# Optimization experiments

Measured on AMD Instinct MI355X. Metric: run time of the kernel, lower is better.

## Reference

```python
import jax, jax.numpy as jnp
import numpy as np

EPS = 1e-5

def _layernorm(x, w, b):
    # x: [B, L, C]; WithBias_LayerNorm over last dim (biased variance)
    mu = jnp.mean(x, axis=-1, keepdims=True)
    var = jnp.mean((x - mu) ** 2, axis=-1, keepdims=True)
    return (x - mu) / jnp.sqrt(var + EPS) * w + b

def _selective_scan(x, x_proj_w, dt_w, A_logs, Ds):
    # x: [B, D, L]  (D = ssm d_inner = 192, N = d_state = 16, R = dt_rank = 6)
    Bsz, D, L = x.shape
    N = A_logs.shape[1]
    R = dt_w.shape[1]
    x_dbl = jnp.einsum('bdl,rd->blr', x, x_proj_w)            # [B, L, R+2N]
    dts_r = x_dbl[..., :R]
    Bs = x_dbl[..., R:R + N]                                   # [B, L, N]
    Cs = x_dbl[..., R + N:]                                    # [B, L, N]
    dts = jax.nn.softplus(jnp.einsum('blr,dr->bld', dts_r, dt_w))  # [B, L, D]
    As = -jnp.exp(A_logs.astype(jnp.float32))                  # [D, N]
    dt_A = jnp.exp(jnp.einsum('bld,dn->bldn', dts, As))        # [B, L, D, N]
    dt_B_x = jnp.einsum('bld,bln,bdl->bldn', dts, Bs, x)       # [B, L, D, N]

    def step(u, inp):
        a, bx, c = inp                                         # [B,D,N],[B,D,N],[B,N]
        u = a * u + bx
        y = jnp.einsum('bdn,bn->bd', u, c)
        return u, y

    u0 = jnp.zeros((Bsz, D, N), dtype=jnp.float32)
    _, ys = jax.lax.scan(step, u0, (jnp.swapaxes(dt_A, 0, 1),
                                     jnp.swapaxes(dt_B_x, 0, 1),
                                     jnp.swapaxes(Cs, 0, 1)))
    y = jnp.swapaxes(ys, 0, 1)                                 # [B, L, D]
    y = y + jnp.einsum('bdl,d->bld', x, Ds.astype(jnp.float32))
    return y


def setup_inputs() -> dict:
    key = jax.random.key(0)
    ks = jax.random.split(key, 12)
    B, C, H, W = 64, 2048, 24, 8
    D_in2, Dssm, N, R = 384, 192, 16, 6
    s = 0.02
    return {
        'feat_map': jax.random.normal(ks[0], (B, C, H, W), jnp.float32),
        'ln_w': jnp.ones((C,), jnp.float32),
        'ln_b': jnp.zeros((C,), jnp.float32),
        'in_w': jax.random.normal(ks[1], (D_in2, C), jnp.float32) * s,
        'in_b': jnp.zeros((D_in2,), jnp.float32),
        'x_proj_w': jax.random.normal(ks[2], (R + 2 * N, Dssm), jnp.float32) * s,
        'dt_w': jax.random.normal(ks[3], (Dssm, R), jnp.float32) * 0.1,
        'A_logs': jnp.log(jnp.broadcast_to(jnp.arange(1, N + 1, dtype=jnp.float32), (Dssm, N))),
        'Ds': jnp.ones((Dssm,), jnp.float32),
        'out_w': jax.random.normal(ks[4], (C, Dssm), jnp.float32) * s,
        'out_b': jnp.zeros((C,), jnp.float32),
        'mo_w': jax.random.normal(ks[5], (C, C), jnp.float32) * s,
        'mo_b': jnp.zeros((C,), jnp.float32),
        'bn_w': jnp.ones((C,), jnp.float32),
        'bn_b': jnp.zeros((C,), jnp.float32),
        'bn_rm': jax.random.normal(ks[6], (C,), jnp.float32) * 0.1,
        'bn_rv': jax.random.uniform(ks[7], (C,), jnp.float32) + 0.5,
    }


def reference(feat_map, ln_w, ln_b, in_w, in_b, x_proj_w, dt_w, A_logs, Ds,
              out_w, out_b, mo_w, mo_b, bn_w, bn_b, bn_rm, bn_rv):
    B, C, H, W = feat_map.shape
    L = H * W
    x3 = feat_map.transpose(0, 2, 3, 1).reshape(B, L, C)       # to_3d
    fm = _layernorm(x3, ln_w, ln_b)                            # normalized feat_map [B, L, C]
    xz = jnp.einsum('blc,oc->blo', fm, in_w) + in_b            # 1x1 conv in_proj
    x, z = jnp.split(xz, 2, axis=-1)                           # each [B, L, 192]
    xd = jnp.swapaxes(x, 1, 2)                                 # [B, D, L]
    yf = _selective_scan(xd, x_proj_w, dt_w, A_logs, Ds)       # [B, L, D]
    yb = _selective_scan(xd[:, :, ::-1], x_proj_w, dt_w, A_logs, Ds)[:, ::-1, :]
    ssm = yf + yb                                              # [B, L, D]
    ssm = ssm * jax.nn.silu(z)
    out = jnp.einsum('bld,cd->blc', ssm, out_w) + out_b        # out_proj 1x1 conv
    out = out + fm                                             # drop_path is identity at eval
    out = jnp.einsum('blc,oc->blo', out, mo_w) + mo_b          # mamba_out conv 1x1
    out = (out - bn_rm) / jnp.sqrt(bn_rv + EPS) * bn_w + bn_b  # BatchNorm (eval)
    out = jax.nn.relu(out)
    return out.reshape(B, H, W, C).transpose(0, 3, 1, 2)
```

## Files before the change

### kernel.cpp

```cpp
#include <hip/hip_runtime.h>
#include <math.h>

#define EPSV 1e-5f


typedef __attribute__((ext_vector_type(8))) __bf16 bf16x8;
typedef __attribute__((ext_vector_type(4))) float f32x4;

__device__ __forceinline__ ushort f2bf(float f) {
  union { float f; unsigned u; } v; v.f = f;
  const unsigned r = v.u + 0x7fffu + ((v.u >> 16) & 1u);
  return (ushort)(r >> 16);
}

#define GLOAD16(G, L) __builtin_amdgcn_global_load_lds( \
    (__attribute__((address_space(1))) void*)(G), \
    (__attribute__((address_space(3))) void*)(L), 16, 0, 0)

__global__ __launch_bounds__(256) void cvt_kernel(
    const float* __restrict__ s, ushort* __restrict__ d, int n)
{
  const int i = (blockIdx.x * 256 + threadIdx.x) * 4;
  if (i + 3 < n) {
    const float4 v = *(const float4*)(s + i);
    ushort4 o;
    o.x = f2bf(v.x); o.y = f2bf(v.y); o.z = f2bf(v.z); o.w = f2bf(v.w);
    *(ushort4*)(d + i) = o;
  }
}

__global__ __launch_bounds__(256) void transpose_w(
    const float* __restrict__ w, ushort* __restrict__ wT)
{
  __shared__ float t[64][65];
  const int c0 = blockIdx.x * 64, d0 = blockIdx.y * 64;
  const int tl = threadIdx.x & 63, tg = threadIdx.x >> 6;
#pragma unroll
  for (int r = 0; r < 16; ++r) {
    const int c = r * 4 + tg;
    t[c][tl] = w[(size_t)(c0 + c) * 192 + d0 + tl];
  }
  __syncthreads();
#pragma unroll
  for (int r = 0; r < 16; ++r) {
    const int d = r * 4 + tg;
    wT[(size_t)(d0 + d) * 2048 + c0 + tl] = f2bf(t[tl][d]);
  }
}

__global__ __launch_bounds__(256) void ln_stats(
    const float* __restrict__ feat, float* __restrict__ sums)
{
  const int b = blockIdx.x, c0 = blockIdx.y * 128;
  const int l = threadIdx.x;
  if (l >= 192) return;
  const float* p = feat + ((size_t)b * 2048 + c0) * 192 + l;
  float s = 0.f, sq = 0.f;
  for (int c = 0; c < 128; ++c) { const float v = p[(size_t)c * 192]; s += v; sq = fmaf(v, v, sq); }
  atomicAdd(&sums[(b * 192 + l) * 2], s);
  atomicAdd(&sums[(b * 192 + l) * 2 + 1], sq);
}

__global__ __launch_bounds__(256) void ln_apply(
    const float* __restrict__ feat, const float* __restrict__ sums,
    const float* __restrict__ lnw, const float* __restrict__ lnb,
    ushort* __restrict__ fm)
{
  __shared__ float tile[64][65];
  __shared__ float smu[64], srs[64];
  const int b = blockIdx.x, c0 = blockIdx.y * 64, l0 = blockIdx.z * 64;
  const int tl = threadIdx.x & 63, tg = threadIdx.x >> 6;
#pragma unroll
  for (int r = 0; r < 16; ++r) {
    const int c = r * 4 + tg;
    tile[c][tl] = feat[((size_t)b * 2048 + c0 + c) * 192 + l0 + tl];
  }
  if (threadIdx.x < 64) {
    const float s  = sums[(b * 192 + l0 + threadIdx.x) * 2];
    const float sq = sums[(b * 192 + l0 + threadIdx.x) * 2 + 1];
    const float mu = s * (1.f / 2048.f);
    smu[threadIdx.x] = mu;
    srs[threadIdx.x] = rsqrtf(sq * (1.f / 2048.f) - mu * mu + EPSV);
  }
  __syncthreads();
  const float w = lnw[c0 + tl], bb = lnb[c0 + tl];
#pragma unroll
  for (int r = 0; r < 16; ++r) {
    const int ll = r * 4 + tg;
    fm[((size_t)(b * 192 + l0 + ll)) * 2048 + c0 + tl] =
        f2bf((tile[tl][ll] - smu[ll]) * srs[ll] * w + bb);
  }
}

__device__ __forceinline__ void mfma_phase(
    const ushort* __restrict__ Ag, int lda,
    const ushort* __restrict__ Bg, int ldb, int K,
    int bm, int bn, int tid, ushort* As, ushort* Bs, f32x4 acc[4][4])
{
  const int lane = tid & 63, wave = tid >> 6;
  const int wm = (wave & 1) << 6, wn = (wave >> 1) << 6;
  const int fr = lane & 15, q = lane >> 4;
  const int r0 = tid >> 2, kc = (tid & 3) << 3;
  const int lb = (tid & 192) * 8;
  for (int k0 = 0; k0 < K; k0 += 32) {
    __syncthreads();
    GLOAD16(Ag + (size_t)(bm + r0) * lda + k0 + kc,      As + lb);
    GLOAD16(Ag + (size_t)(bm + 64 + r0) * lda + k0 + kc, As + 2048 + lb);
    GLOAD16(Bg + (size_t)(bn + r0) * ldb + k0 + kc,      Bs + lb);
    GLOAD16(Bg + (size_t)(bn + 64 + r0) * ldb + k0 + kc, Bs + 2048 + lb);
    __syncthreads();
    bf16x8 af[4], bfr[4];
#pragma unroll
    for (int i = 0; i < 4; ++i) {
      af[i]  = *(const bf16x8*)&As[(wm + i * 16 + fr) * 32 + q * 8];
      bfr[i] = *(const bf16x8*)&Bs[(wn + i * 16 + fr) * 32 + q * 8];
    }
#pragma unroll
    for (int i = 0; i < 4; ++i)
#pragma unroll
      for (int j = 0; j < 4; ++j)
        acc[i][j] = __builtin_amdgcn_mfma_f32_16x16x32_bf16(af[i], bfr[j], acc[i][j], 0, 0, 0);
  }
}

template<int MODE>
__global__ __launch_bounds__(256) void mfma_gemm(
    const ushort* __restrict__ A1, const ushort* __restrict__ B1,
    const ushort* __restrict__ A2, const ushort* __restrict__ B2,
    const float* __restrict__ p0, const float* __restrict__ p1,
    float* __restrict__ out, ushort* __restrict__ outb)
{
  __shared__ ushort As[4096], Bs[4096];
  const int tid = threadIdx.x;
  const int bm = blockIdx.y * 128, bn = blockIdx.x * 128;
  f32x4 acc[4][4];
#pragma unroll
  for (int i = 0; i < 4; ++i)
#pragma unroll
    for (int j = 0; j < 4; ++j) acc[i][j] = (f32x4)(0.f);

  mfma_phase(A1, 2048, B1, 2048, 2048, bm, bn, tid, As, Bs, acc);
  if (MODE == 1)
    mfma_phase(A2, 192, B2, 192, 192, bm, bn, tid, As, Bs, acc);

  const int lane = tid & 63, wave = tid >> 6;
  const int wm = (wave & 1) << 6, wn = (wave >> 1) << 6;
  const int fr = lane & 15, q = lane >> 4;
  if (MODE == 0) {
#pragma unroll
    for (int mi = 0; mi < 4; ++mi) {
      const int m0 = bm + wm + mi * 16 + q * 4;
#pragma unroll
      for (int ni = 0; ni < 4; ++ni) {
        const int n = bn + wn + ni * 16 + fr;
        const float bias = p0[n];
#pragma unroll
        for (int r = 0; r < 4; ++r)
          out[(size_t)(m0 + r) * 384 + n] = acc[mi][ni][r] + bias;
      }
    }
  } else if (MODE == 1) {
#pragma unroll
    for (int mi = 0; mi < 4; ++mi) {
      const int m0 = bm + wm + mi * 16 + q * 4;
      const int b = m0 / 192, l0 = m0 - b * 192;
#pragma unroll
      for (int ni = 0; ni < 4; ++ni) {
        const int n = bn + wn + ni * 16 + fr;
        const float sc = p0[n], sh = p1[n];
        float4 o;
        o.x = fmaxf(fmaf(acc[mi][ni][0], sc, sh), 0.f);
        o.y = fmaxf(fmaf(acc[mi][ni][1], sc, sh), 0.f);
        o.z = fmaxf(fmaf(acc[mi][ni][2], sc, sh), 0.f);
        o.w = fmaxf(fmaf(acc[mi][ni][3], sc, sh), 0.f);
        *(float4*)(out + ((size_t)b * 2048 + n) * 192 + l0) = o;
      }
    }
  } else {
#pragma unroll
    for (int mi = 0; mi < 4; ++mi) {
      const int m0 = bm + wm + mi * 16 + q * 4;
#pragma unroll
      for (int ni = 0; ni < 4; ++ni) {
        const int n = bn + wn + ni * 16 + fr;
        if (n < 192) {
#pragma unroll
          for (int r = 0; r < 4; ++r)
            outb[(size_t)(m0 + r) * 192 + n] = f2bf(acc[mi][ni][r]);
        }
      }
    }
  }
}

__global__ __launch_bounds__(64) void xproj_kernel(
    const float* __restrict__ xz, const float* __restrict__ xpw,
    const float* __restrict__ dtw, float* __restrict__ dts,
    float* __restrict__ Bsb, float* __restrict__ Csb)
{
  const int m = blockIdx.x, tid = threadIdx.x;
  __shared__ float xrow[192];
  __shared__ float xdbl[38];
  const float* src = xz + (size_t)m * 384;
#pragma unroll
  for (int i = 0; i < 3; ++i) xrow[tid + i * 64] = src[tid + i * 64];
  __syncthreads();
  if (tid < 38) {
    float a = 0.f;
    const float* wr = xpw + tid * 192;
    for (int d = 0; d < 192; ++d) a = fmaf(xrow[d], wr[d], a);
    xdbl[tid] = a;
  }
  __syncthreads();
  if (tid < 16) Bsb[(size_t)m * 16 + tid] = xdbl[6 + tid];
  else if (tid < 32) Csb[(size_t)m * 16 + (tid - 16)] = xdbl[22 + (tid - 16)];
#pragma unroll
  for (int i = 0; i < 3; ++i) {
    const int d = tid + i * 64;
    const float* w = dtw + d * 6;
    float a = xdbl[0] * w[0] + xdbl[1] * w[1] + xdbl[2] * w[2]
            + xdbl[3] * w[3] + xdbl[4] * w[4] + xdbl[5] * w[5];
    dts[(size_t)m * 192 + d] = (a > 20.f) ? a : log1pf(__expf(a));
  }
}

__global__ __launch_bounds__(256) void scan_kernel(
    const float* __restrict__ xz, const float* __restrict__ dts,
    const float* __restrict__ Bsb, const float* __restrict__ Csb,
    const float* __restrict__ A_logs, const float* __restrict__ Ds,
    ushort* __restrict__ ssm)
{
  __shared__ float s_dt[3072], s_x[3072], s_B[3072], s_C[3072], s_y[3072];
  const int tid = threadIdx.x;
  const int b = blockIdx.x / 12, dblk = blockIdx.x - b * 12;
  const int d0 = dblk * 16;
  const size_t rbase = (size_t)b * 192;
  for (int i = tid; i < 768; i += 256) {
    const int l = i >> 2, j = (i & 3) << 2;
    const size_t row = rbase + l;
    ((float4*)s_dt)[i] = *(const float4*)(dts + row * 192 + d0 + j);
    ((float4*)s_x)[i]  = *(const float4*)(xz  + row * 384 + d0 + j);
    ((float4*)s_B)[i]  = *(const float4*)(Bsb + row * 16 + j);
    ((float4*)s_C)[i]  = *(const float4*)(Csb + row * 16 + j);
  }
  __syncthreads();
  const int n = tid & 15, dl = tid >> 4;
  const float Acoef = -expf(A_logs[(d0 + dl) * 16 + n]);
  float u = 0.f;
#pragma unroll 4
  for (int l = 0; l < 192; ++l) {
    const float dt = s_dt[l * 16 + dl];
    const float c  = dt * s_B[l * 16 + n] * s_x[l * 16 + dl];
    const float a  = __expf(dt * Acoef);
    u = fmaf(a, u, c);
    float y = u * s_C[l * 16 + n];
    y += __shfl_xor(y, 1, 16); y += __shfl_xor(y, 2, 16);
    y += __shfl_xor(y, 4, 16); y += __shfl_xor(y, 8, 16);
    if (n == 0) s_y[l * 16 + dl] = y;
  }
  u = 0.f;
#pragma unroll 4
  for (int l = 191; l >= 0; --l) {
    const float dt = s_dt[l * 16 + dl];
    const float c  = dt * s_B[l * 16 + n] * s_x[l * 16 + dl];
    const float a  = __expf(dt * Acoef);
    u = fmaf(a, u, c);
    float y = u * s_C[l * 16 + n];
    y += __shfl_xor(y, 1, 16); y += __shfl_xor(y, 2, 16);
    y += __shfl_xor(y, 4, 16); y += __shfl_xor(y, 8, 16);
    if (n == 0) s_y[l * 16 + dl] += y;
  }
  __syncthreads();
  for (int i = tid; i < 768; i += 256) {
    const int l = i >> 2, j = (i & 3) << 2;
    const size_t row = rbase + l;
    const float4 y4 = ((const float4*)s_y)[i];
    const float4 x4 = ((const float4*)s_x)[i];
    const float4 z4 = *(const float4*)(xz + row * 384 + 192 + d0 + j);
    const float4 D4 = *(const float4*)(Ds + d0 + j);
    ushort4 o;
    o.x = f2bf((y4.x + 2.f * x4.x * D4.x) * (z4.x / (1.f + __expf(-z4.x))));
    o.y = f2bf((y4.y + 2.f * x4.y * D4.y) * (z4.y / (1.f + __expf(-z4.y))));
    o.z = f2bf((y4.z + 2.f * x4.z * D4.z) * (z4.z / (1.f + __expf(-z4.z))));
    o.w = f2bf((y4.w + 2.f * x4.w * D4.w) * (z4.w / (1.f + __expf(-z4.w))));
    *(ushort4*)(ssm + row * 192 + d0 + j) = o;
  }
}

__global__ __launch_bounds__(64) void prep_kernel(
    const float* __restrict__ mo_w, const float* __restrict__ mo_b,
    const float* __restrict__ out_b,
    const float* __restrict__ bn_w, const float* __restrict__ bn_b,
    const float* __restrict__ bn_rm, const float* __restrict__ bn_rv,
    float* __restrict__ scale, float* __restrict__ shift)
{
  const int o = blockIdx.x, tid = threadIdx.x;
  float s = 0.f;
  for (int c = tid; c < 2048; c += 64) s = fmaf(mo_w[(size_t)o * 2048 + c], out_b[c], s);
#pragma unroll
  for (int off = 32; off > 0; off >>= 1) s += __shfl_down(s, off, 64);
  if (tid == 0) {
    const float b2 = s + mo_b[o];
    const float sc = bn_w[o] * rsqrtf(bn_rv[o] + EPSV);
    scale[o] = sc;
    shift[o] = (b2 - bn_rm[o]) * sc + bn_b[o];
  }
}

extern "C" void kernel_launch(void* const* d_in, const int* in_sizes, int n_in,
                              void* d_out, int out_size, void* d_ws, size_t ws_size,
                              hipStream_t stream) {
  const float* feat  = (const float*)d_in[0];
  const float* ln_w  = (const float*)d_in[1];
  const float* ln_b  = (const float*)d_in[2];
  const float* in_w  = (const float*)d_in[3];
  const float* in_b  = (const float*)d_in[4];
  const float* xpw   = (const float*)d_in[5];
  const float* dtw   = (const float*)d_in[6];
  const float* A_logs= (const float*)d_in[7];
  const float* Ds    = (const float*)d_in[8];
  const float* out_w = (const float*)d_in[9];
  const float* out_b = (const float*)d_in[10];
  const float* mo_w  = (const float*)d_in[11];
  const float* mo_b  = (const float*)d_in[12];
  const float* bn_w  = (const float*)d_in[13];
  const float* bn_b  = (const float*)d_in[14];
  const float* bn_rm = (const float*)d_in[15];
  const float* bn_rv = (const float*)d_in[16];
  float* out = (float*)d_out;

  uint8_t* p = (uint8_t*)d_ws;
  ushort* fm_b  = (ushort*)p; p += (size_t)12288 * 2048 * 2;
  float*  xz    = (float*)p;  p += (size_t)12288 * 384 * 4;
  float*  dts   = (float*)p;  p += (size_t)12288 * 192 * 4;
  float*  Bsb   = (float*)p;  p += (size_t)12288 * 16 * 4;
  float*  Csb   = (float*)p;  p += (size_t)12288 * 16 * 4;
  ushort* ssm_b = (ushort*)p; p += (size_t)12288 * 192 * 2;
  ushort* W2b   = (ushort*)p; p += (size_t)2048 * 192 * 2;
  ushort* owT_b = (ushort*)p; p += (size_t)256 * 2048 * 2;
  ushort* mo_wb = (ushort*)p; p += (size_t)2048 * 2048 * 2;
  ushort* in_wb = (ushort*)p; p += (size_t)384 * 2048 * 2;
  float*  scale = (float*)p;  p += 2048 * 4;
  float*  shift = (float*)p;  p += 2048 * 4;
  float*  sums  = (float*)p;  p += (size_t)64 * 192 * 2 * 4;
  if ((size_t)(p - (uint8_t*)d_ws) > ws_size) return;

  cvt_kernel<<<4096, 256, 0, stream>>>(mo_w, mo_wb, 2048 * 2048);
  cvt_kernel<<<768, 256, 0, stream>>>(in_w, in_wb, 384 * 2048);
  hipMemsetAsync(owT_b, 0, (size_t)256 * 2048 * 2, stream);
  transpose_w<<<dim3(32, 3), 256, 0, stream>>>(out_w, owT_b);

  hipMemsetAsync(sums, 0, (size_t)64 * 192 * 2 * 4, stream);
  ln_stats<<<dim3(64, 16), 256, 0, stream>>>(feat, sums);
  ln_apply<<<dim3(64, 32, 3), 256, 0, stream>>>(feat, sums, ln_w, ln_b, fm_b);

  mfma_gemm<0><<<dim3(3, 96), 256, 0, stream>>>(
      fm_b, in_wb, nullptr, nullptr, in_b, nullptr, xz, nullptr);

  xproj_kernel<<<12288, 64, 0, stream>>>(xz, xpw, dtw, dts, Bsb, Csb);
  scan_kernel<<<768, 256, 0, stream>>>(xz, dts, Bsb, Csb, A_logs, Ds, ssm_b);

  mfma_gemm<2><<<dim3(2, 16), 256, 0, stream>>>(
      mo_wb, owT_b, nullptr, nullptr, nullptr, nullptr, nullptr, W2b);
  prep_kernel<<<2048, 64, 0, stream>>>(mo_w, mo_b, out_b, bn_w, bn_b, bn_rm, bn_rv, scale, shift);

  mfma_gemm<1><<<dim3(16, 96), 256, 0, stream>>>(
      fm_b, mo_wb, ssm_b, W2b, scale, shift, out, nullptr);
}
```

Baseline: 717.3 us.

## Replace final fused GEMM with larger-tile double-buffered MFMA kernel

The final 12288x2048x2240 GEMM (fm·mo_w plus ssm·W2) moves from a 128x128 single-buffered kernel to a dedicated 192x256 tile kernel with 512 threads. It uses global_load_lds prefetch two K-steps ahead into double-buffered, XOR-swizzled LDS, and raises wave priority around the MFMA bursts. The aim is more data reuse per tile, less LDS bank conflicting, and overlap of loads with compute. In exchange it uses much more LDS and registers per block, which may limit occupancy, and the hand-written waitcnt and barrier schedule is fragile.

```diff
diff --git a/kernel.cpp b/kernel.cpp
--- a/kernel.cpp
+++ b/kernel.cpp
@@ -126,8 +126,7 @@
 template<int MODE>
 __global__ __launch_bounds__(256) void mfma_gemm(
     const ushort* __restrict__ A1, const ushort* __restrict__ B1,
-    const ushort* __restrict__ A2, const ushort* __restrict__ B2,
-    const float* __restrict__ p0, const float* __restrict__ p1,
+    const float* __restrict__ p0,
     float* __restrict__ out, ushort* __restrict__ outb)
 {
   __shared__ ushort As[4096], Bs[4096];
@@ -140,8 +139,6 @@
     for (int j = 0; j < 4; ++j) acc[i][j] = (f32x4)(0.f);
 
   mfma_phase(A1, 2048, B1, 2048, 2048, bm, bn, tid, As, Bs, acc);
-  if (MODE == 1)
-    mfma_phase(A2, 192, B2, 192, 192, bm, bn, tid, As, Bs, acc);
 
   const int lane = tid & 63, wave = tid >> 6;
   const int wm = (wave & 1) << 6, wn = (wave >> 1) << 6;
@@ -159,23 +156,6 @@
           out[(size_t)(m0 + r) * 384 + n] = acc[mi][ni][r] + bias;
       }
     }
-  } else if (MODE == 1) {
-#pragma unroll
-    for (int mi = 0; mi < 4; ++mi) {
-      const int m0 = bm + wm + mi * 16 + q * 4;
-      const int b = m0 / 192, l0 = m0 - b * 192;
-#pragma unroll
-      for (int ni = 0; ni < 4; ++ni) {
-        const int n = bn + wn + ni * 16 + fr;
-        const float sc = p0[n], sh = p1[n];
-        float4 o;
-        o.x = fmaxf(fmaf(acc[mi][ni][0], sc, sh), 0.f);
-        o.y = fmaxf(fmaf(acc[mi][ni][1], sc, sh), 0.f);
-        o.z = fmaxf(fmaf(acc[mi][ni][2], sc, sh), 0.f);
-        o.w = fmaxf(fmaf(acc[mi][ni][3], sc, sh), 0.f);
-        *(float4*)(out + ((size_t)b * 2048 + n) * 192 + l0) = o;
-      }
-    }
   } else {
 #pragma unroll
     for (int mi = 0; mi < 4; ++mi) {
@@ -189,6 +169,123 @@
             outb[(size_t)(m0 + r) * 192 + n] = f2bf(acc[mi][ni][r]);
         }
       }
+    }
+  }
+}
+
+
+__device__ __forceinline__ void stage7(
+    const ushort* __restrict__ Ag, int lda,
+    const ushort* __restrict__ Bg, int ldb, int k0,
+    int bm, int bn, int tid, ushort* Asl, ushort* Bsl)
+{
+  const int w = tid >> 6, l = tid & 63;
+#pragma unroll
+  for (int c = 0; c < 3; ++c) {
+    const int LC = c * 512 + w * 64 + l;
+    const int row = LC >> 3, sc = (LC & 7) ^ (row & 7);
+    GLOAD16(Ag + (size_t)(bm + row) * lda + k0 + sc * 8, Asl + c * 4096 + w * 512);
+  }
+#pragma unroll
+  for (int c = 0; c < 4; ++c) {
+    const int LC = c * 512 + w * 64 + l;
+    const int row = LC >> 3, sc = (LC & 7) ^ (row & 7);
+    GLOAD16(Bg + (size_t)(bn + row) * ldb + k0 + sc * 8, Bsl + c * 4096 + w * 512);
+  }
+}
+
+__global__ __launch_bounds__(512, 2) void mfma_gemm_big(
+    const ushort* __restrict__ fmw,  const ushort* __restrict__ mow,
+    const ushort* __restrict__ ssmb, const ushort* __restrict__ w2b,
+    const float* __restrict__ scale, const float* __restrict__ shift,
+    float* __restrict__ out)
+{
+  __shared__ ushort As[2 * 12288];
+  __shared__ ushort Bs[2 * 16384];
+  const int tid = threadIdx.x;
+  const int flat = blockIdx.x;
+  const int bx = flat & 7, by = flat >> 3;
+  const int bm = by * 192, bn = bx * 256;
+
+  const int lane = tid & 63, wave = tid >> 6;
+  const int wr = wave >> 2, wc = wave & 3;
+  const int fr = lane & 15, q = lane >> 4;
+
+  constexpr int NT = 35;
+
+  f32x4 acc[6][4];
+#pragma unroll
+  for (int i = 0; i < 6; ++i)
+#pragma unroll
+    for (int j = 0; j < 4; ++j) acc[i][j] = (f32x4)(0.f);
+
+  stage7(fmw, 2048, mow, 2048, 0,  bm, bn, tid, As, Bs);
+  stage7(fmw, 2048, mow, 2048, 64, bm, bn, tid, As + 12288, Bs + 16384);
+  asm volatile("s_waitcnt vmcnt(7)" ::: "memory");
+  asm volatile("" ::: "memory");
+  __builtin_amdgcn_s_barrier();
+  asm volatile("" ::: "memory");
+
+  for (int kt = 0; kt < NT; ++kt) {
+    const int cur = kt & 1;
+    const ushort* Ab = As + cur * 12288;
+    const ushort* Bb = Bs + cur * 16384;
+    bf16x8 bfr[2][4];
+#pragma unroll
+    for (int ph = 0; ph < 4; ++ph) {
+      const int mh = ph >> 1, ks = ph & 1;
+      const int kswz = (((ks << 2) + q) ^ (fr & 7)) << 3;
+      bf16x8 af[3];
+#pragma unroll
+      for (int mi = 0; mi < 3; ++mi)
+        af[mi] = *(const bf16x8*)&Ab[(wr * 96 + (mh * 3 + mi) * 16 + fr) * 64 + kswz];
+      if (ph < 2) {
+#pragma unroll
+        for (int ni = 0; ni < 4; ++ni)
+          bfr[ks][ni] = *(const bf16x8*)&Bb[(wc * 64 + ni * 16 + fr) * 64 + kswz];
+      }
+      __builtin_amdgcn_s_barrier();
+      __builtin_amdgcn_s_setprio(1);
+#pragma unroll
+      for (int mi = 0; mi < 3; ++mi)
+#pragma unroll
+        for (int ni = 0; ni < 4; ++ni)
+          acc[mh * 3 + mi][ni] = __builtin_amdgcn_mfma_f32_16x16x32_bf16(
+              af[mi], bfr[ks][ni], acc[mh * 3 + mi][ni], 0, 0, 0);
+      __builtin_amdgcn_s_setprio(0);
+      __builtin_amdgcn_s_barrier();
+    }
+    const int nk = kt + 2;
+    if (nk < NT) {
+      if (nk < 32)
+        stage7(fmw, 2048, mow, 2048, nk * 64, bm, bn, tid,
+               As + cur * 12288, Bs + cur * 16384);
+      else
+        stage7(ssmb, 192, w2b, 192, (nk - 32) * 64, bm, bn, tid,
+               As + cur * 12288, Bs + cur * 16384);
+      asm volatile("s_waitcnt vmcnt(7)" ::: "memory");
+    } else if (kt + 1 < NT) {
+      asm volatile("s_waitcnt vmcnt(0)" ::: "memory");
+    }
+    asm volatile("" ::: "memory");
+    __builtin_amdgcn_s_barrier();
+    asm volatile("" ::: "memory");
+  }
+
+#pragma unroll
+  for (int mi = 0; mi < 6; ++mi) {
+    const int m0 = bm + wr * 96 + mi * 16 + q * 4;
+    const int b = m0 / 192, l0 = m0 - b * 192;
+#pragma unroll
+    for (int ni = 0; ni < 4; ++ni) {
+      const int n = bn + wc * 64 + ni * 16 + fr;
+      const float sc = scale[n], sh = shift[n];
+      float4 o;
+      o.x = fmaxf(fmaf(acc[mi][ni][0], sc, sh), 0.f);
+      o.y = fmaxf(fmaf(acc[mi][ni][1], sc, sh), 0.f);
+      o.z = fmaxf(fmaf(acc[mi][ni][2], sc, sh), 0.f);
+      o.w = fmaxf(fmaf(acc[mi][ni][3], sc, sh), 0.f);
+      *(float4*)(out + ((size_t)b * 2048 + n) * 192 + l0) = o;
     }
   }
 }
@@ -355,15 +452,14 @@
   ln_apply<<<dim3(64, 32, 3), 256, 0, stream>>>(feat, sums, ln_w, ln_b, fm_b);
 
   mfma_gemm<0><<<dim3(3, 96), 256, 0, stream>>>(
-      fm_b, in_wb, nullptr, nullptr, in_b, nullptr, xz, nullptr);
+      fm_b, in_wb, in_b, xz, nullptr);
 
   xproj_kernel<<<12288, 64, 0, stream>>>(xz, xpw, dtw, dts, Bsb, Csb);
   scan_kernel<<<768, 256, 0, stream>>>(xz, dts, Bsb, Csb, A_logs, Ds, ssm_b);
 
   mfma_gemm<2><<<dim3(2, 16), 256, 0, stream>>>(
-      mo_wb, owT_b, nullptr, nullptr, nullptr, nullptr, nullptr, W2b);
+      mo_wb, owT_b, nullptr, nullptr, W2b);
   prep_kernel<<<2048, 64, 0, stream>>>(mo_w, mo_b, out_b, bn_w, bn_b, bn_rm, bn_rv, scale, shift);
 
-  mfma_gemm<1><<<dim3(16, 96), 256, 0, stream>>>(
-      fm_b, mo_wb, ssm_b, W2b, scale, shift, out, nullptr);
-}
+  mfma_gemm_big<<<512, 512, 0, stream>>>(fm_b, mo_wb, ssm_b, W2b, scale, shift, out);
+}
```

After: 711.8 us. Within noise of the previous version (-0.8%).

## Replace final fused GEMM with 256x256-tile pipelined MFMA kernel

Applied to the files above, without the earlier changes.

The final GEMM, which combines fm·mo_w with ssm·W2 and applies the BN/ReLU epilogue, now runs in a new 512-thread kernel. Each block computes a 256x256 tile with 64-wide K steps, double-buffered LDS fed by async global_load_lds, XOR-swizzled LDS rows, and prefetch interleaved with the MFMA phases under raised wave priority. To keep K a multiple of 64, the ssm and W2 buffers are padded from 192 to 256 columns, and the extra columns are zero-filled by a memset. The aim is more operand reuse and overlap of memory traffic with MFMA, at the cost of higher register and LDS use (128KB LDS per block) and the extra memset.

```diff
diff --git a/kernel.cpp b/kernel.cpp
--- a/kernel.cpp
+++ b/kernel.cpp
@@ -16,6 +16,10 @@
 #define GLOAD16(G, L) __builtin_amdgcn_global_load_lds( \
     (__attribute__((address_space(1))) void*)(G), \
     (__attribute__((address_space(3))) void*)(L), 16, 0, 0)
+
+#define BAR() do { asm volatile("" ::: "memory"); \
+  __builtin_amdgcn_s_barrier(); \
+  asm volatile("" ::: "memory"); } while (0)
 
 __global__ __launch_bounds__(256) void cvt_kernel(
     const float* __restrict__ s, ushort* __restrict__ d, int n)
@@ -126,8 +130,7 @@
 template<int MODE>
 __global__ __launch_bounds__(256) void mfma_gemm(
     const ushort* __restrict__ A1, const ushort* __restrict__ B1,
-    const ushort* __restrict__ A2, const ushort* __restrict__ B2,
-    const float* __restrict__ p0, const float* __restrict__ p1,
+    const float* __restrict__ p0,
     float* __restrict__ out, ushort* __restrict__ outb)
 {
   __shared__ ushort As[4096], Bs[4096];
@@ -140,8 +143,6 @@
     for (int j = 0; j < 4; ++j) acc[i][j] = (f32x4)(0.f);
 
   mfma_phase(A1, 2048, B1, 2048, 2048, bm, bn, tid, As, Bs, acc);
-  if (MODE == 1)
-    mfma_phase(A2, 192, B2, 192, 192, bm, bn, tid, As, Bs, acc);
 
   const int lane = tid & 63, wave = tid >> 6;
   const int wm = (wave & 1) << 6, wn = (wave >> 1) << 6;
@@ -159,36 +160,137 @@
           out[(size_t)(m0 + r) * 384 + n] = acc[mi][ni][r] + bias;
       }
     }
-  } else if (MODE == 1) {
+  } else {
 #pragma unroll
     for (int mi = 0; mi < 4; ++mi) {
       const int m0 = bm + wm + mi * 16 + q * 4;
-      const int b = m0 / 192, l0 = m0 - b * 192;
 #pragma unroll
       for (int ni = 0; ni < 4; ++ni) {
         const int n = bn + wn + ni * 16 + fr;
-        const float sc = p0[n], sh = p1[n];
-        float4 o;
-        o.x = fmaxf(fmaf(acc[mi][ni][0], sc, sh), 0.f);
-        o.y = fmaxf(fmaf(acc[mi][ni][1], sc, sh), 0.f);
-        o.z = fmaxf(fmaf(acc[mi][ni][2], sc, sh), 0.f);
-        o.w = fmaxf(fmaf(acc[mi][ni][3], sc, sh), 0.f);
-        *(float4*)(out + ((size_t)b * 2048 + n) * 192 + l0) = o;
+#pragma unroll
+        for (int r = 0; r < 4; ++r)
+          outb[(size_t)(m0 + r) * 256 + n] = f2bf(acc[mi][ni][r]);
       }
     }
-  } else {
-#pragma unroll
-    for (int mi = 0; mi < 4; ++mi) {
-      const int m0 = bm + wm + mi * 16 + q * 4;
-#pragma unroll
-      for (int ni = 0; ni < 4; ++ni) {
-        const int n = bn + wn + ni * 16 + fr;
-        if (n < 192) {
-#pragma unroll
-          for (int r = 0; r < 4; ++r)
-            outb[(size_t)(m0 + r) * 192 + n] = f2bf(acc[mi][ni][r]);
+  }
+}
+
+
+__device__ __forceinline__ void stage_half(
+    int t, int kind,
+    int bm, int bn, int tid,
+    const ushort* __restrict__ fmw, const ushort* __restrict__ mow,
+    const ushort* __restrict__ ssmb, const ushort* __restrict__ w2b,
+    ushort* As, ushort* Bs)
+{
+  const bool isA = (kind < 2);
+  const ushort* G; int ld, k0;
+  if (t < 32) { G = isA ? fmw : mow;  ld = 2048; k0 = t * 64; }
+  else        { G = isA ? ssmb : w2b; ld = 256;  k0 = (t - 32) * 64; }
+  const int p0 = isA ? bm : bn;
+  ushort* L = (isA ? As : Bs) + (t & 1) * 16384 + (kind & 1) * 8192;
+  const int w = tid >> 6, l = tid & 63;
+#pragma unroll
+  for (int j = 0; j < 2; ++j) {
+    const int LC = j * 512 + w * 64 + l;
+    const int row = (kind & 1) * 128 + (LC >> 3);
+    const int sc = (LC & 7) ^ (row & 7);
+    GLOAD16(G + (size_t)(p0 + row) * ld + k0 + sc * 8, L + j * 4096 + w * 512);
+  }
+}
+
+__global__ __launch_bounds__(512, 2) void mfma_gemm_big(
+    const ushort* __restrict__ fmw,  const ushort* __restrict__ mow,
+    const ushort* __restrict__ ssmb, const ushort* __restrict__ w2b,
+    const float* __restrict__ scale, const float* __restrict__ shift,
+    float* __restrict__ out)
+{
+  __shared__ ushort As[2 * 16384];
+  __shared__ ushort Bs[2 * 16384];
+  const int tid = threadIdx.x;
+  const int flat = blockIdx.x;
+  const int bx = flat & 7, by = flat >> 3;
+  const int bm = by * 256, bn = bx * 256;
+
+  const int lane = tid & 63, wave = tid >> 6;
+  const int wr = wave >> 2, wc = wave & 3;
+  const int fr = lane & 15, q = lane >> 4;
+
+  constexpr int NT = 36;
+
+  f32x4 acc[8][4];
+#pragma unroll
+  for (int i = 0; i < 8; ++i)
+#pragma unroll
+    for (int j = 0; j < 4; ++j) acc[i][j] = (f32x4)(0.f);
+
+  stage_half(0, 0, bm, bn, tid, fmw, mow, ssmb, w2b, As, Bs);
+  stage_half(0, 1, bm, bn, tid, fmw, mow, ssmb, w2b, As, Bs);
+  stage_half(0, 2, bm, bn, tid, fmw, mow, ssmb, w2b, As, Bs);
+  stage_half(0, 3, bm, bn, tid, fmw, mow, ssmb, w2b, As, Bs);
+  stage_half(1, 2, bm, bn, tid, fmw, mow, ssmb, w2b, As, Bs);
+  stage_half(1, 3, bm, bn, tid, fmw, mow, ssmb, w2b, As, Bs);
+  asm volatile("s_waitcnt vmcnt(4)" ::: "memory");
+  BAR();
+
+  for (int t = 0; t < NT; ++t) {
+    const ushort* Ab = As + (t & 1) * 16384;
+    const ushort* Bb = Bs + (t & 1) * 16384;
+    bf16x8 bfr[4];
+#pragma unroll
+    for (int ph = 0; ph < 4; ++ph) {
+      const int ks = ph >> 1, mh = ph & 1;
+      const int kswz = (((ks << 2) + q) ^ (fr & 7)) << 3;
+      bf16x8 af[4];
+#pragma unroll
+      for (int mi = 0; mi < 4; ++mi)
+        af[mi] = *(const bf16x8*)&Ab[(wr * 128 + mh * 64 + mi * 16 + fr) * 64 + kswz];
+      if (mh == 0) {
+#pragma unroll
+        for (int ni = 0; ni < 4; ++ni)
+          bfr[ni] = *(const bf16x8*)&Bb[(wc * 64 + ni * 16 + fr) * 64 + kswz];
+      }
+      if (ph == 0) {
+        if (t + 1 < NT) stage_half(t + 1, 0, bm, bn, tid, fmw, mow, ssmb, w2b, As, Bs);
+      } else if (ph == 1) {
+        if (t + 1 < NT) stage_half(t + 1, 1, bm, bn, tid, fmw, mow, ssmb, w2b, As, Bs);
+      } else if (ph == 3) {
+        if (t + 2 < NT) {
+          stage_half(t + 2, 2, bm, bn, tid, fmw, mow, ssmb, w2b, As, Bs);
+          stage_half(t + 2, 3, bm, bn, tid, fmw, mow, ssmb, w2b, As, Bs);
         }
       }
+      BAR();
+      __builtin_amdgcn_s_setprio(1);
+#pragma unroll
+      for (int mi = 0; mi < 4; ++mi)
+#pragma unroll
+        for (int ni = 0; ni < 4; ++ni)
+          acc[mh * 4 + mi][ni] = __builtin_amdgcn_mfma_f32_16x16x32_bf16(
+              af[mi], bfr[ni], acc[mh * 4 + mi][ni], 0, 0, 0);
+      __builtin_amdgcn_s_setprio(0);
+      if (ph == 3) {
+        if (t <= 33) asm volatile("s_waitcnt vmcnt(4)" ::: "memory");
+        else if (t == 34) asm volatile("s_waitcnt vmcnt(0)" ::: "memory");
+      }
+      BAR();
+    }
+  }
+
+#pragma unroll
+  for (int mi = 0; mi < 8; ++mi) {
+    const int m0 = bm + wr * 128 + mi * 16 + q * 4;
+    const int b = m0 / 192, l0 = m0 - b * 192;
+#pragma unroll
+    for (int ni = 0; ni < 4; ++ni) {
+      const int n = bn + wc * 64 + ni * 16 + fr;
+      const float sc = scale[n], sh = shift[n];
+      float4 o;
+      o.x = fmaxf(fmaf(acc[mi][ni][0], sc, sh), 0.f);
+      o.y = fmaxf(fmaf(acc[mi][ni][1], sc, sh), 0.f);
+      o.z = fmaxf(fmaf(acc[mi][ni][2], sc, sh), 0.f);
+      o.w = fmaxf(fmaf(acc[mi][ni][3], sc, sh), 0.f);
+      *(float4*)(out + ((size_t)b * 2048 + n) * 192 + l0) = o;
     }
   }
 }
@@ -283,7 +385,7 @@
     o.y = f2bf((y4.y + 2.f * x4.y * D4.y) * (z4.y / (1.f + __expf(-z4.y))));
     o.z = f2bf((y4.z + 2.f * x4.z * D4.z) * (z4.z / (1.f + __expf(-z4.z))));
     o.w = f2bf((y4.w + 2.f * x4.w * D4.w) * (z4.w / (1.f + __expf(-z4.w))));
-    *(ushort4*)(ssm + row * 192 + d0 + j) = o;
+    *(ushort4*)(ssm + row * 256 + d0 + j) = o;
   }
 }
 
@@ -335,8 +437,8 @@
   float*  dts   = (float*)p;  p += (size_t)12288 * 192 * 4;
   float*  Bsb   = (float*)p;  p += (size_t)12288 * 16 * 4;
   float*  Csb   = (float*)p;  p += (size_t)12288 * 16 * 4;
-  ushort* ssm_b = (ushort*)p; p += (size_t)12288 * 192 * 2;
-  ushort* W2b   = (ushort*)p; p += (size_t)2048 * 192 * 2;
+  ushort* ssm_b = (ushort*)p; p += (size_t)12288 * 256 * 2;
+  ushort* W2b   = (ushort*)p; p += (size_t)2048 * 256 * 2;
   ushort* owT_b = (ushort*)p; p += (size_t)256 * 2048 * 2;
   ushort* mo_wb = (ushort*)p; p += (size_t)2048 * 2048 * 2;
   ushort* in_wb = (ushort*)p; p += (size_t)384 * 2048 * 2;
@@ -348,6 +450,7 @@
   cvt_kernel<<<4096, 256, 0, stream>>>(mo_w, mo_wb, 2048 * 2048);
   cvt_kernel<<<768, 256, 0, stream>>>(in_w, in_wb, 384 * 2048);
   hipMemsetAsync(owT_b, 0, (size_t)256 * 2048 * 2, stream);
+  hipMemsetAsync(ssm_b, 0, (size_t)12288 * 256 * 2, stream);
   transpose_w<<<dim3(32, 3), 256, 0, stream>>>(out_w, owT_b);
 
   hipMemsetAsync(sums, 0, (size_t)64 * 192 * 2 * 4, stream);
@@ -355,15 +458,14 @@
   ln_apply<<<dim3(64, 32, 3), 256, 0, stream>>>(feat, sums, ln_w, ln_b, fm_b);
 
   mfma_gemm<0><<<dim3(3, 96), 256, 0, stream>>>(
-      fm_b, in_wb, nullptr, nullptr, in_b, nullptr, xz, nullptr);
+      fm_b, in_wb, in_b, xz, nullptr);
 
   xproj_kernel<<<12288, 64, 0, stream>>>(xz, xpw, dtw, dts, Bsb, Csb);
   scan_kernel<<<768, 256, 0, stream>>>(xz, dts, Bsb, Csb, A_logs, Ds, ssm_b);
 
   mfma_gemm<2><<<dim3(2, 16), 256, 0, stream>>>(
-      mo_wb, owT_b, nullptr, nullptr, nullptr, nullptr, nullptr, W2b);
+      mo_wb, owT_b, nullptr, nullptr, W2b);
   prep_kernel<<<2048, 64, 0, stream>>>(mo_w, mo_b, out_b, bn_w, bn_b, bn_rm, bn_rv, scale, shift);
 
-  mfma_gemm<1><<<dim3(16, 96), 256, 0, stream>>>(
-      fm_b, mo_wb, ssm_b, W2b, scale, shift, out, nullptr);
-}
+  mfma_gemm_big<<<384, 512, 0, stream>>>(fm_b, mo_wb, ssm_b, W2b, scale, shift, out);
+}
```

Result: faster. 701.2 us (-2.3%).
